# Optimization experiments

Hardware: AMD Instinct MI355X
Metric: run time of the kernel (lower is better)

Reference implementation:

```python
import jax, jax.numpy as jnp
import numpy as np
import math

B, S, H = 8, 2048, 512
DI, DS, DC, DR = 1024, 16, 4, 32   # d_inner, d_state, d_conv, dt_rank
NL, V, NLAB = 8, 32000, 2


def _ln(x, g, b, eps=1e-12):
    mu = jnp.mean(x, -1, keepdims=True)
    var = jnp.mean((x - mu) ** 2, -1, keepdims=True)
    return g * (x - mu) / jnp.sqrt(var + eps) + b


def _gelu_new(x):
    return 0.5 * x * (1.0 + jnp.tanh(np.sqrt(2.0 / np.pi).astype(np.float32) * (x + 0.044715 * x ** 3)))


def _mamba(xin, Wi, cw, cb, Wx, Wdt, bdt, Alog, Dp, Wo):
    # xin: [B,S,H]
    Bb, L, _ = xin.shape
    xz = jnp.einsum('blh,eh->ble', xin, Wi)          # [B,L,2*DI]
    x, z = xz[..., :DI], xz[..., DI:]
    # causal depthwise conv1d, kernel DC, padding DC-1 truncated to L
    xp = jnp.pad(x, ((0, 0), (DC - 1, 0), (0, 0)))
    xc = sum(cw[:, k] * xp[:, k:k + L, :] for k in range(DC)) + cb
    x = jax.nn.silu(xc)
    xdb = jnp.einsum('bld,rd->blr', x, Wx)           # [B,L,DR+2*DS]
    dt = jax.nn.softplus(jnp.einsum('blr,dr->bld', xdb[..., :DR], Wdt) + bdt)
    Bm = xdb[..., DR:DR + DS]
    Cm = xdb[..., DR + DS:]
    A = -jnp.exp(Alog)                               # [DI,DS]

    def step(h, t):
        dt_t, B_t, C_t, x_t = t                      # [B,DI],[B,DS],[B,DS],[B,DI]
        dA = jnp.exp(dt_t[:, :, None] * A)           # [B,DI,DS]
        h = dA * h + (dt_t * x_t)[:, :, None] * B_t[:, None, :]
        return h, jnp.einsum('bdn,bn->bd', h, C_t)

    tm = lambda a: jnp.swapaxes(a, 0, 1)             # time-major
    h0 = jnp.zeros((Bb, DI, DS), x.dtype)
    _, ys = jax.lax.scan(step, h0, (tm(dt), tm(Bm), tm(Cm), tm(x)))
    y = jnp.swapaxes(ys, 0, 1) + Dp * x
    y = y * jax.nn.silu(z)
    return jnp.einsum('bld,hd->blh', y, Wo)


def _forward(input_ids, gate, age_sex, word_emb, pos_emb2, pe, emb_ln_g, emb_ln_b,
             in_proj_w, conv_w, conv_b, x_proj_w, dt_proj_w, dt_proj_b, A_log, D_param,
             out_proj_w, blk_ln_g, blk_ln_b, dense2_w, dense2_b, male_fc_w, male_fc_b,
             gn_g, gn_b, head_w, head_b):
    emb_in = word_emb[input_ids]                                  # [B,S,H]
    emb = pos_emb2[None, :S] * emb_in + pe[None, :S]
    emb = _ln(emb, emb_ln_g, emb_ln_b)
    seq = gate[:, :, None] * emb
    for l in range(NL):
        h = _mamba(seq, in_proj_w[l], conv_w[l], conv_b[l], x_proj_w[l],
                   dt_proj_w[l], dt_proj_b[l], A_log[l], D_param[l], out_proj_w[l])
        seq = gate[:, :, None] * _ln(h + seq, blk_ln_g[l], blk_ln_b[l])
    # ClassificationHead4
    x = seq * gate[:, :, None]
    pooled = jnp.max(x, axis=1)                                   # AdaptiveMaxPool2d((1,H)) == max over seq
    feat = _gelu_new(pooled @ dense2_w.T + dense2_b)              # [B,512]
    style = jax.nn.elu(age_sex @ male_fc_w.T + male_fc_b)         # [B,1024]
    fg = feat.reshape(feat.shape[0], 4, H // 4)                   # GroupNorm(4, 512)
    mu = jnp.mean(fg, -1, keepdims=True)
    var = jnp.mean((fg - mu) ** 2, -1, keepdims=True)
    gn = ((fg - mu) / jnp.sqrt(var + 1e-5)).reshape(feat.shape[0], H) * gn_g + gn_b
    feature = (1.0 + style[:, :H]) * gn + style[:, H:]
    logits = feature @ head_w.T + head_b
    return logits, gate, feature


def setup_inputs() -> dict:
    key = jax.random.key(0)
    ks = jax.random.split(key, 24)
    n = lambda k, sh, s=0.02: jax.random.normal(k, sh, dtype=jnp.float32) * s
    # sinusoidal position buffer
    pos = np.arange(S)[:, None].astype(np.float32)
    div = np.exp(np.arange(0, H, 2).astype(np.float32) * (-math.log(10000.0) / H))
    pe = np.zeros((S, H), np.float32)
    pe[:, 0::2] = np.sin(pos * div)
    pe[:, 1::2] = np.cos(pos * div)
    A_log = jnp.log(jnp.broadcast_to(jnp.arange(1, DS + 1, dtype=jnp.float32), (NL, DI, DS)))
    return {
        'input_ids': jax.random.randint(ks[0], (B, S), 0, V),
        'gate': jax.random.uniform(ks[1], (B, S), dtype=jnp.float32),
        'age_sex': jax.random.normal(ks[2], (B, 2), dtype=jnp.float32),
        'word_emb': n(ks[3], (V, H)),
        'pos_emb2': 1.0 + n(ks[4], (S, H)),
        'pe': jnp.asarray(pe),
        'emb_ln_g': jnp.ones((H,), jnp.float32),
        'emb_ln_b': jnp.zeros((H,), jnp.float32),
        'in_proj_w': n(ks[5], (NL, 2 * DI, H)),
        'conv_w': n(ks[6], (NL, DI, DC), 0.1),
        'conv_b': jnp.zeros((NL, DI), jnp.float32),
        'x_proj_w': n(ks[7], (NL, DR + 2 * DS, DI)),
        'dt_proj_w': n(ks[8], (NL, DI, DR), 0.1),
        'dt_proj_b': n(ks[9], (NL, DI), 0.1),
        'A_log': A_log,
        'D_param': jnp.ones((NL, DI), jnp.float32),
        'out_proj_w': n(ks[10], (NL, H, DI)),
        'blk_ln_g': jnp.ones((NL, H), jnp.float32),
        'blk_ln_b': jnp.zeros((NL, H), jnp.float32),
        'dense2_w': n(ks[11], (512, H)),
        'dense2_b': jnp.zeros((512,), jnp.float32),
        'male_fc_w': n(ks[12], (2 * H, 2)),
        'male_fc_b': jnp.zeros((2 * H,), jnp.float32),
        'gn_g': jnp.ones((512,), jnp.float32),
        'gn_b': jnp.zeros((512,), jnp.float32),
        'head_w': n(ks[13], (NLAB, 512)),
        'head_b': jnp.zeros((NLAB,), jnp.float32),
    }


def reference(input_ids, gate, age_sex, word_emb, pos_emb2, pe, emb_ln_g, emb_ln_b,
              in_proj_w, conv_w, conv_b, x_proj_w, dt_proj_w, dt_proj_b, A_log, D_param,
              out_proj_w, blk_ln_g, blk_ln_b, dense2_w, dense2_b, male_fc_w, male_fc_b,
              gn_g, gn_b, head_w, head_b):
    return _forward(input_ids, gate, age_sex, word_emb, pos_emb2, pe, emb_ln_g, emb_ln_b,
                    in_proj_w, conv_w, conv_b, x_proj_w, dt_proj_w, dt_proj_b, A_log, D_param,
                    out_proj_w, blk_ln_g, blk_ln_b, dense2_w, dense2_b, male_fc_w, male_fc_b,
                    gn_g, gn_b, head_w, head_b)
```

## Files before the change

kernel.cpp:

```cpp
#include <hip/hip_runtime.h>
#include <hip/hip_bf16.h>
#include <hip/hip_fp16.h>
#include <math.h>

#define B_ 8
#define S_ 2048
#define H_ 512
#define DI_ 1024
#define DS_ 16
#define DC_ 4
#define DR_ 32
#define NL_ 8
#define PF_ 4

typedef __hip_bfloat16 bf16;
typedef short bf16x8 __attribute__((ext_vector_type(8)));
typedef float f32x4 __attribute__((ext_vector_type(4)));
typedef float f32x16 __attribute__((ext_vector_type(16)));
typedef unsigned short u16x8 __attribute__((ext_vector_type(8)));

static __device__ __forceinline__ float wred_sum(float v) {
#pragma unroll
  for (int o = 32; o; o >>= 1) v += __shfl_down(v, o, 64);
  return v;
}
static __device__ __forceinline__ float bf2f(unsigned short u) {
  return __uint_as_float(((unsigned)u) << 16);
}
static __device__ __forceinline__ float h2f(unsigned short u) {
  __half_raw r;
  r.x = u;
  return __half2float(r);
}
static __device__ __forceinline__ void st1(float* p, float v) { *p = v; }
static __device__ __forceinline__ void st1(bf16* p, float v) { *p = __float2bfloat16(v); }
static __device__ __forceinline__ void st1(__half* p, float v) { *p = __float2half(v); }
static __device__ __forceinline__ unsigned short f2bfu(float v) {
  bf16 b = __float2bfloat16(v);
  unsigned short u;
  __builtin_memcpy(&u, &b, 2);
  return u;
}

static __device__ __forceinline__ void gl_lds16(const unsigned short* g,
                                                unsigned short* l) {
  __builtin_amdgcn_global_load_lds(
      (const __attribute__((address_space(1))) void*)g,
      (__attribute__((address_space(3))) void*)l, 16, 0, 0);
}

static __device__ __forceinline__ f32x16 ld_c16(const float* p) {
  return *(const __attribute__((address_space(4))) f32x16*)p;
}

template <bool FAST>
static __device__ __forceinline__ void decay16(float dt, const float* A,
                                               float* p) {
  if constexpr (FAST) {
    float q = __expf(-dt);
    float q2 = q * q, q3 = q2 * q, q4 = q2 * q2;
    p[0] = q; p[1] = q2; p[2] = q3; p[3] = q4;
    p[4] = q4 * q; p[5] = q4 * q2; p[6] = q4 * q3;
    float q8 = q4 * q4;
    p[7] = q8;
#pragma unroll
    for (int n = 0; n < 8; n++) p[8 + n] = q8 * p[n];
  } else {
#pragma unroll
    for (int n = 0; n < 16; n++) p[n] = __expf(dt * A[n]);
  }
}

template <int BM, int BN, int ACT, typename TC>
__global__ void __launch_bounds__((BM / 64) * (BN / 64) * 64) k_mfma(
    const unsigned short* __restrict__ X, int lda,
    const unsigned short* __restrict__ W, int ldb,
    const float* __restrict__ bias, TC* __restrict__ C, long ldc, int K,
    unsigned short* __restrict__ dtbf) {
  constexpr int NW = (BM / 64) * (BN / 64);
  constexpr int WN = BN / 64;
  constexpr int SEGS = (BM + BN) / 16;
  __shared__ unsigned short As[BM * 32];
  __shared__ unsigned short Bs[BN * 32];
  int tid = threadIdx.x;
  int wave = tid >> 6, lane = tid & 63;
  int wm = wave / WN, wn = wave % WN;
  long row0 = (long)blockIdx.y * BM;
  long col0 = (long)blockIdx.x * BN;
  int srow = lane >> 2;
  int kchunk = (lane & 3) ^ (srow & 3);
  f32x4 acc[4][4] = {};
  for (int k0 = 0; k0 < K; k0 += 32) {
#pragma unroll
    for (int s = wave; s < SEGS; s += NW) {
      if (s < BM / 16) {
        const unsigned short* g =
            X + (row0 + s * 16 + srow) * (long)lda + k0 + kchunk * 8;
        gl_lds16(g, &As[s * 16 * 32]);
      } else {
        int s2 = s - BM / 16;
        const unsigned short* g =
            W + (col0 + s2 * 16 + srow) * (long)ldb + k0 + kchunk * 8;
        gl_lds16(g, &Bs[s2 * 16 * 32]);
      }
    }
    __syncthreads();
    int fr = lane & 15;
    int slot = (lane >> 4) ^ (lane & 3);
    bf16x8 af[4], bfr[4];
#pragma unroll
    for (int i = 0; i < 4; i++)
      af[i] = *(const bf16x8*)&As[(wm * 64 + i * 16 + fr) * 32 + slot * 8];
#pragma unroll
    for (int j = 0; j < 4; j++)
      bfr[j] = *(const bf16x8*)&Bs[(wn * 64 + j * 16 + fr) * 32 + slot * 8];
#pragma unroll
    for (int i = 0; i < 4; i++)
#pragma unroll
      for (int j = 0; j < 4; j++)
        acc[i][j] = __builtin_amdgcn_mfma_f32_16x16x32_bf16(af[i], bfr[j],
                                                            acc[i][j], 0, 0, 0);
    __syncthreads();
  }
#pragma unroll
  for (int i = 0; i < 4; i++) {
#pragma unroll
    for (int j = 0; j < 4; j++) {
      long rbase = row0 + wm * 64 + i * 16 + ((lane >> 4) << 2);
      long c = col0 + wn * 64 + j * 16 + (lane & 15);
#pragma unroll
      for (int reg = 0; reg < 4; reg++) {
        float v = acc[i][j][reg];
        long r = rbase + reg;
        if constexpr (ACT == 2) {
          if (c < 32) st1((bf16*)&dtbf[r * 32 + c], v);
          else st1((float*)&C[r * ldc + (c - 32)], v);
        } else {
          if constexpr (ACT == 1) {
            v += bias[c];
            v = fmaxf(v, 0.f) + log1pf(__expf(-fabsf(v)));
          }
          st1(&C[r * ldc + c], v);
        }
      }
    }
  }
}

__global__ void k_convert4(const float* __restrict__ s0, int n0,
                           const float* __restrict__ s1, int n1,
                           const float* __restrict__ s2, int n2,
                           const float* __restrict__ s3, int n3,
                           bf16* __restrict__ d0, bf16* __restrict__ d1,
                           bf16* __restrict__ d2, bf16* __restrict__ d3) {
  int i = blockIdx.x * 256 + threadIdx.x;
  int t0 = n0 >> 2, t1 = t0 + (n1 >> 2), t2 = t1 + (n2 >> 2), t3 = t2 + (n3 >> 2);
  const float* s;
  bf16* d;
  int loc;
  if (i < t0) { s = s0; d = d0; loc = i; }
  else if (i < t1) { s = s1; d = d1; loc = i - t0; }
  else if (i < t2) { s = s2; d = d2; loc = i - t1; }
  else if (i < t3) { s = s3; d = d3; loc = i - t2; }
  else return;
  float4 v = ((const float4*)s)[loc];
  bf16* o = d + (long)loc * 4;
  st1(o + 0, v.x); st1(o + 1, v.y); st1(o + 2, v.z); st1(o + 3, v.w);
}

__global__ void k_embed(const int* __restrict__ ids, const float* __restrict__ gate,
                        const float* __restrict__ wemb, const float* __restrict__ pos2,
                        const float* __restrict__ pe, const float* __restrict__ g,
                        const float* __restrict__ bta, bf16* __restrict__ seq) {
  int row = blockIdx.x;
  int s = row % S_;
  int t = threadIdx.x;
  int id = ids[row];
  float v[2];
#pragma unroll
  for (int i = 0; i < 2; i++) {
    int h = t + i * 256;
    v[i] = pos2[s * H_ + h] * wemb[(long)id * H_ + h] + pe[s * H_ + h];
  }
  float lsum = v[0] + v[1];
  float lsq = v[0] * v[0] + v[1] * v[1];
  __shared__ float smA[4], smB[4];
  int lane = t & 63, w = t >> 6;
  lsum = wred_sum(lsum);
  lsq = wred_sum(lsq);
  if (!lane) { smA[w] = lsum; smB[w] = lsq; }
  __syncthreads();
  float tot = smA[0] + smA[1] + smA[2] + smA[3];
  float totq = smB[0] + smB[1] + smB[2] + smB[3];
  float mu = tot * (1.f / H_);
  float var = totq * (1.f / H_) - mu * mu;
  float inv = rsqrtf(fmaxf(var, 0.f) + 1e-12f);
  float gt = gate[row];
#pragma unroll
  for (int i = 0; i < 2; i++) {
    int h = t + i * 256;
    st1(&seq[(long)row * H_ + h], gt * (g[h] * (v[i] - mu) * inv + bta[h]));
  }
}

__global__ void __launch_bounds__(256) k_conv(const bf16* __restrict__ xz,
                                              const float* __restrict__ cw,
                                              const float* __restrict__ cb,
                                              bf16* __restrict__ xc) {
  __shared__ float cwL[8 * 512];
  __shared__ float cbL[8 * 128];
  int tid = threadIdx.x;
#pragma unroll
  for (int m = 0; m < 4; m++) {
    int dd = m * 256 + tid;
    float4 v = ((const float4*)cw)[dd];
    int e = dd & 7, a = dd >> 3;
    *(float4*)&cwL[e * 512 + (((a + e) & 127) << 2)] = v;
  }
  {
    float4 v = ((const float4*)cb)[tid];
#pragma unroll
    for (int m = 0; m < 4; m++) {
      int dd = tid * 4 + m;
      int e = dd & 7, a = dd >> 3;
      cbL[e * 128 + ((a + e) & 127)] = ((const float*)&v)[m];
    }
  }
  __syncthreads();
  long idx = ((long)blockIdx.x * 256 + tid) * 8;
  int d0 = (int)(idx & 1023);
  int A = d0 >> 3;
  long bt = idx >> 10;
  int t = (int)(bt & 2047);
  const unsigned short* xbase = (const unsigned short*)xz + (bt - t) * 2048 + d0;
  f32x4 wk[8];
  float acc[8];
#pragma unroll
  for (int e = 0; e < 8; e++) {
    wk[e] = *(const f32x4*)&cwL[e * 512 + (((A + e) & 127) << 2)];
    acc[e] = cbL[e * 128 + ((A + e) & 127)];
  }
#pragma unroll
  for (int k = 0; k < 4; k++) {
    int ts = t + k - 3;
    if (ts >= 0) {
      u16x8 xv = *(const u16x8*)&xbase[(long)ts * 2048];
#pragma unroll
      for (int e = 0; e < 8; e++) acc[e] += wk[e][k] * bf2f(xv[e]);
    }
  }
  u16x8 ov;
#pragma unroll
  for (int e = 0; e < 8; e++) {
    float s = acc[e] / (1.f + __expf(-acc[e]));
    ov[e] = f2bfu(s);
  }
  *(u16x8*)((unsigned short*)xc + idx) = ov;
}

__global__ void __launch_bounds__(64) k_scan(
    bf16* __restrict__ xzb, const bf16* __restrict__ xc,
    const float* __restrict__ xdb, const float* __restrict__ Alog,
    const float* __restrict__ Dp) {
  int idx = blockIdx.x * 64 + threadIdx.x;
  int half = idx & 1;
  int p = idx >> 1;
  int d = p & 1023;
  int b = p >> 10;
  int n0 = half * 8;
  float A[8];
#pragma unroll
  for (int n = 0; n < 8; n++) A[n] = -__expf(Alog[d * 16 + n0 + n]);
  float Dd = Dp[d];
  float h[8] = {0, 0, 0, 0, 0, 0, 0, 0};
  const __half* dtb = (const __half*)xzb + (long)b * S_ * 2048 + d;
  const unsigned short* xb = (const unsigned short*)xc + (long)b * S_ * DI_ + d;
  const unsigned short* zb = (const unsigned short*)xzb + (long)b * S_ * 2048 + DI_ + d;
  const float* bcb = xdb + (long)b * S_ * 32 + n0;
  bf16* yb = xzb + (long)b * S_ * 2048 + d;
  float dt_c = __half2float(dtb[0]);
  float x_c = bf2f(xb[0]);
  float z_c = bf2f(zb[0]);
  float Bc[8], Cc[8];
#pragma unroll
  for (int n = 0; n < 8; n++) { Bc[n] = bcb[n]; Cc[n] = bcb[16 + n]; }
  for (int t = 0; t < S_; t++) {
    float dt_n = 0.f, x_n = 0.f, z_n = 0.f, Bn[8], Cn[8];
#pragma unroll
    for (int n = 0; n < 8; n++) { Bn[n] = 0.f; Cn[n] = 0.f; }
    if (t + 1 < S_) {
      long o = (long)(t + 1);
      dt_n = __half2float(dtb[o * 2048]);
      x_n = bf2f(xb[o * DI_]);
      z_n = bf2f(zb[o * 2048]);
      const float* bc = bcb + o * 32;
#pragma unroll
      for (int n = 0; n < 8; n++) { Bn[n] = bc[n]; Cn[n] = bc[16 + n]; }
    }
    float dx = dt_c * x_c;
    float yacc = 0.f;
#pragma unroll
    for (int n = 0; n < 8; n++) {
      float hn = __expf(dt_c * A[n]) * h[n] + dx * Bc[n];
      h[n] = hn;
      yacc += hn * Cc[n];
    }
    yacc += __shfl_xor(yacc, 1, 64);
    if (!half) {
      float sz = z_c / (1.f + __expf(-z_c));
      st1(&yb[(long)t * 2048], (yacc + Dd * x_c) * sz);
    }
    dt_c = dt_n; x_c = x_n; z_c = z_n;
#pragma unroll
    for (int n = 0; n < 8; n++) { Bc[n] = Bn[n]; Cc[n] = Cn[n]; }
  }
}

template <int LCv, bool FAST>
static __device__ __forceinline__ void scanA_body16(
    const __half* dtb, const unsigned short* xb, const float* bcb,
    const float* A, int t0, float* h, float& sd) {
  float dtv[PF_], xv[PF_];
  f32x16 bv[2];
#pragma unroll
  for (int i = 0; i < PF_; i++) {
    long o = t0 + i;
    dtv[i] = __half2float(dtb[o * 2048]);
    xv[i] = bf2f(xb[o * DI_]);
  }
#pragma unroll
  for (int i = 0; i < 2; i++) bv[i] = ld_c16(bcb + (long)(t0 + i) * 32);
  for (int t = 0; t < LCv; t += PF_) {
#pragma unroll
    for (int u = 0; u < PF_; u++) {
      float dt_c = dtv[u], x_c = xv[u];
      f32x16 Bv = bv[u & 1];
      long ov = t0 + t + u + PF_;
      dtv[u] = __half2float(dtb[ov * 2048]);
      xv[u] = bf2f(xb[ov * DI_]);
      bv[u & 1] = ld_c16(bcb + (long)(t0 + t + u + 2) * 32);
      sd += dt_c;
      float dx = dt_c * x_c;
      float p[16];
      decay16<FAST>(dt_c, A, p);
#pragma unroll
      for (int n = 0; n < 16; n++) h[n] = p[n] * h[n] + dx * Bv[n];
    }
  }
}

template <int NCv>
__global__ void __launch_bounds__(256) k_scanA(
    const bf16* __restrict__ xzb, const bf16* __restrict__ xc,
    const float* __restrict__ xdb, const float* __restrict__ Alog,
    __half* __restrict__ hf, __half* __restrict__ sdt) {
  constexpr int LCv = S_ / NCv;
  int bx = blockIdx.x;
  int c = bx >> 5;
  int b = (bx >> 2) & 7;
  int d = ((bx & 3) << 8) + threadIdx.x;
  int p = (b << 10) + d;
  float A[16];
  bool fast = true;
#pragma unroll
  for (int n = 0; n < 16; n++) {
    A[n] = -__expf(Alog[d * 16 + n]);
    fast = fast && (fabsf(A[n] + (float)(n + 1)) < 1e-3f);
  }
  const __half* dtb = (const __half*)xzb + (long)b * S_ * 2048 + d;
  const unsigned short* xb = (const unsigned short*)xc + (long)b * S_ * DI_ + d;
  const float* bcb = xdb + (long)b * S_ * 32;
  int t0 = c * LCv;
  float h[16] = {};
  float sd = 0.f;
  if (fast) scanA_body16<LCv, true>(dtb, xb, bcb, A, t0, h, sd);
  else scanA_body16<LCv, false>(dtb, xb, bcb, A, t0, h, sd);
  __half* ho = hf + ((long)c * 8192 + p) * 16;
#pragma unroll
  for (int n = 0; n < 16; n++) st1(&ho[n], h[n]);
  st1(&sdt[c * 8192 + p], sd);
}

template <int NCv>
__global__ void __launch_bounds__(256) k_scanB(
    const float* __restrict__ Alog, __half* __restrict__ hf,
    const __half* __restrict__ sdt) {
  constexpr int M = NCv - 1;
  int i = blockIdx.x * 256 + threadIdx.x;
  int n = i & 15;
  int p = i >> 4;
  int d = p & 1023;
  float An = -__expf(Alog[d * 16 + n]);
  float sdv[8], hjv[8];
#pragma unroll
  for (int k = 0; k < 8; k++) {
    int j = k < M ? k : M - 1;
    sdv[k] = h2f(((const unsigned short*)sdt)[j * 8192 + p]);
    hjv[k] = h2f(((const unsigned short*)hf)[((long)j * 8192 + p) * 16 + n]);
  }
  float H = 0.f;
  for (int j = 0; j < M; j++) {
    float sd = sdv[j & 7], hj = hjv[j & 7];
    int jn = j + 8;
    if (jn > M - 1) jn = M - 1;
    sdv[j & 7] = h2f(((const unsigned short*)sdt)[jn * 8192 + p]);
    hjv[j & 7] = h2f(((const unsigned short*)hf)[((long)jn * 8192 + p) * 16 + n]);
    H = __expf(sd * An) * H + hj;
    st1(&hf[((long)j * 8192 + p) * 16 + n], H);
  }
}

template <bool FAST>
static __device__ __forceinline__ void step16(float dt, float x, float z,
                                              const f32x16& B, const f32x16& C,
                                              const float* A, float Dd,
                                              float* h, bf16* yout) {
  float p[16];
  decay16<FAST>(dt, A, p);
  float dx = dt * x;
  float y0 = 0.f, y1 = 0.f, y2 = 0.f, y3 = 0.f;
#pragma unroll
  for (int n = 0; n < 16; n += 4) {
    float h0 = p[n + 0] * h[n + 0] + dx * B[n + 0];
    float h1 = p[n + 1] * h[n + 1] + dx * B[n + 1];
    float h2 = p[n + 2] * h[n + 2] + dx * B[n + 2];
    float h3 = p[n + 3] * h[n + 3] + dx * B[n + 3];
    h[n + 0] = h0; h[n + 1] = h1; h[n + 2] = h2; h[n + 3] = h3;
    y0 += h0 * C[n + 0];
    y1 += h1 * C[n + 1];
    y2 += h2 * C[n + 2];
    y3 += h3 * C[n + 3];
  }
  float yacc = (y0 + y1) + (y2 + y3);
  float sz = z / (1.f + __expf(-z));
  st1(yout, (yacc + Dd * x) * sz);
}

template <int LCv, bool FAST>
static __device__ __forceinline__ void scanC_body16(
    const __half* dtb, const unsigned short* xb, const unsigned short* zb,
    const float* bcb, bf16* yb, const float* A, int t0, float Dd, float* h) {
  float dtv[PF_], xv[PF_], zv[PF_];
  f32x16 bv[2], cv[2];
#pragma unroll
  for (int i = 0; i < PF_; i++) {
    long o = t0 + i;
    dtv[i] = __half2float(dtb[o * 2048]);
    xv[i] = bf2f(xb[o * DI_]);
    zv[i] = bf2f(zb[o * 2048]);
  }
#pragma unroll
  for (int i = 0; i < 2; i++) {
    bv[i] = ld_c16(bcb + (long)(t0 + i) * 32);
    cv[i] = ld_c16(bcb + (long)(t0 + i) * 32 + 16);
  }
  for (int t = 0; t < LCv - PF_; t += PF_) {
#pragma unroll
    for (int u = 0; u < PF_; u++) {
      float dt_c = dtv[u], x_c = xv[u], z_c = zv[u];
      f32x16 Bv = bv[u & 1], Cv = cv[u & 1];
      long ov = t0 + t + u + PF_;
      dtv[u] = __half2float(dtb[ov * 2048]);
      xv[u] = bf2f(xb[ov * DI_]);
      zv[u] = bf2f(zb[ov * 2048]);
      long os = t0 + t + u + 2;
      bv[u & 1] = ld_c16(bcb + os * 32);
      cv[u & 1] = ld_c16(bcb + os * 32 + 16);
      step16<FAST>(dt_c, x_c, z_c, Bv, Cv, A, Dd, h,
                   yb + (long)(t0 + t + u) * 2048);
    }
  }
#pragma unroll
  for (int u = 0; u < PF_; u++) {
    int tt = LCv - PF_ + u;
    f32x16 Bv, Cv;
    if (u < 2) {
      Bv = bv[u];
      Cv = cv[u];
    } else {
      Bv = ld_c16(bcb + (long)(t0 + tt) * 32);
      Cv = ld_c16(bcb + (long)(t0 + tt) * 32 + 16);
    }
    step16<FAST>(dtv[u], xv[u], zv[u], Bv, Cv, A, Dd, h,
                 yb + (long)(t0 + tt) * 2048);
  }
}

template <int NCv>
__global__ void __launch_bounds__(256) k_scanC(
    bf16* __restrict__ xzb, const bf16* __restrict__ xc,
    const float* __restrict__ xdb, const float* __restrict__ Alog,
    const float* __restrict__ Dp, const __half* __restrict__ hf,
    const __half* __restrict__ sdt) {
  constexpr int LCv = S_ / NCv;
  int bx = blockIdx.x;
  int c = bx >> 5;
  int b = (bx >> 2) & 7;
  int d = ((bx & 3) << 8) + threadIdx.x;
  int p = (b << 10) + d;
  float A[16];
  bool fast = true;
#pragma unroll
  for (int n = 0; n < 16; n++) {
    A[n] = -__expf(Alog[d * 16 + n]);
    fast = fast && (fabsf(A[n] + (float)(n + 1)) < 1e-3f);
  }
  float Dd = Dp[d];
  float h[16] = {};
  if (c > 0) {
    const unsigned short* hs =
        (const unsigned short*)hf + ((long)(c - 1) * 8192 + p) * 16;
    u16x8 a = *(const u16x8*)hs;
    u16x8 b2 = *(const u16x8*)(hs + 8);
#pragma unroll
    for (int n = 0; n < 8; n++) { h[n] = h2f(a[n]); h[8 + n] = h2f(b2[n]); }
  }
  const __half* dtb = (const __half*)xzb + (long)b * S_ * 2048 + d;
  const unsigned short* xb = (const unsigned short*)xc + (long)b * S_ * DI_ + d;
  const unsigned short* zb =
      (const unsigned short*)xzb + (long)b * S_ * 2048 + DI_ + d;
  const float* bcb = xdb + (long)b * S_ * 32;
  bf16* yb = xzb + (long)b * S_ * 2048 + d;
  int t0 = c * LCv;
  if (fast) scanC_body16<LCv, true>(dtb, xb, zb, bcb, yb, A, t0, Dd, h);
  else scanC_body16<LCv, false>(dtb, xb, zb, bcb, yb, A, t0, Dd, h);
}

__global__ void k_resid_ln(const bf16* __restrict__ hb, const float* __restrict__ gate,
                           const float* __restrict__ g, const float* __restrict__ bta,
                           bf16* __restrict__ seq) {
  int row = blockIdx.x;
  int t = threadIdx.x;
  float v[2];
#pragma unroll
  for (int i = 0; i < 2; i++) {
    int h = t + i * 256;
    v[i] = bf2f(((const unsigned short*)hb)[(long)row * H_ + h]) +
           bf2f(((const unsigned short*)seq)[(long)row * H_ + h]);
  }
  float lsum = v[0] + v[1];
  float lsq = v[0] * v[0] + v[1] * v[1];
  __shared__ float smA[4], smB[4];
  int lane = t & 63, w = t >> 6;
  lsum = wred_sum(lsum);
  lsq = wred_sum(lsq);
  if (!lane) { smA[w] = lsum; smB[w] = lsq; }
  __syncthreads();
  float tot = smA[0] + smA[1] + smA[2] + smA[3];
  float totq = smB[0] + smB[1] + smB[2] + smB[3];
  float mu = tot * (1.f / H_);
  float var = totq * (1.f / H_) - mu * mu;
  float inv = rsqrtf(fmaxf(var, 0.f) + 1e-12f);
  float gt = gate[row];
#pragma unroll
  for (int i = 0; i < 2; i++) {
    int h = t + i * 256;
    st1(&seq[(long)row * H_ + h], gt * (g[h] * (v[i] - mu) * inv + bta[h]));
  }
}

__global__ void __launch_bounds__(64) k_pool1(const bf16* __restrict__ seq,
                                              const float* __restrict__ gate,
                                              float* __restrict__ part) {
  int blk = blockIdx.x;
  int b = blk >> 5, c = blk & 31;
  int h0 = threadIdx.x * 8;
  float m[8];
#pragma unroll
  for (int e = 0; e < 8; e++) m[e] = -3.4e38f;
  long r0 = (long)b * S_ + c * 64;
#pragma unroll 4
  for (int i = 0; i < 64; i++) {
    long r = r0 + i;
    u16x8 v = *(const u16x8*)&((const unsigned short*)seq)[r * H_ + h0];
    float g = gate[r];
#pragma unroll
    for (int e = 0; e < 8; e++) m[e] = fmaxf(m[e], bf2f(v[e]) * g);
  }
  float* o = part + ((long)b * 32 + c) * H_ + h0;
#pragma unroll
  for (int e = 0; e < 8; e++) o[e] = m[e];
}
__global__ void k_pool2(const float* __restrict__ part, float* __restrict__ pooled) {
  int idx = blockIdx.x * 256 + threadIdx.x;
  int b = idx >> 9, h = idx & 511;
  float m = -3.4e38f;
#pragma unroll
  for (int c = 0; c < 32; c++) m = fmaxf(m, part[((long)b * 32 + c) * H_ + h]);
  pooled[idx] = m;
}

__global__ void k_feat(const float* __restrict__ pooled, const float* __restrict__ W2,
                       const float* __restrict__ b2, float* __restrict__ feat) {
  int b = blockIdx.x;
  int j = threadIdx.x;
  __shared__ float ps[512];
  ps[j] = pooled[b * 512 + j];
  __syncthreads();
  float acc = b2[j];
  const float4* wr = (const float4*)(W2 + (long)j * 512);
  const float4* p4 = (const float4*)ps;
  for (int k = 0; k < 128; k++) {
    float4 a = p4[k], bb = wr[k];
    acc += a.x * bb.x + a.y * bb.y + a.z * bb.z + a.w * bb.w;
  }
  float x = acc;
  float u = 0.7978845608028654f * (x + 0.044715f * x * x * x);
  feat[b * 512 + j] = 0.5f * x * (1.f + tanhf(u));
}

__global__ void k_head(const float* __restrict__ feat, const float* __restrict__ age_sex,
                       const float* __restrict__ mw, const float* __restrict__ mb,
                       const float* __restrict__ gng, const float* __restrict__ gnb,
                       const float* __restrict__ hw, const float* __restrict__ hb,
                       float* __restrict__ out) {
  int b = blockIdx.x;
  int j = threadIdx.x;
  float f = feat[b * 512 + j];
  __shared__ float sA[8], sB[8];
  int lane = j & 63, w = j >> 6;
  float s1 = wred_sum(f);
  float s2 = wred_sum(f * f);
  if (!lane) { sA[w] = s1; sB[w] = s2; }
  __syncthreads();
  int g = j >> 7;
  float tot = sA[2 * g] + sA[2 * g + 1];
  float totq = sB[2 * g] + sB[2 * g + 1];
  float mu = tot * (1.f / 128.f);
  float var = totq * (1.f / 128.f) - mu * mu;
  float gn = (f - mu) * rsqrtf(fmaxf(var, 0.f) + 1e-5f) * gng[j] + gnb[j];
  float a0 = age_sex[b * 2], a1 = age_sex[b * 2 + 1];
  float sa = a0 * mw[j * 2] + a1 * mw[j * 2 + 1] + mb[j];
  sa = sa > 0.f ? sa : (__expf(sa) - 1.f);
  int j2 = 512 + j;
  float sb = a0 * mw[j2 * 2] + a1 * mw[j2 * 2 + 1] + mb[j2];
  sb = sb > 0.f ? sb : (__expf(sb) - 1.f);
  float feature = (1.f + sa) * gn + sb;
  out[16 + 16384 + b * 512 + j] = feature;
  float l0 = feature * hw[j];
  float l1 = feature * hw[512 + j];
  __syncthreads();
  l0 = wred_sum(l0);
  l1 = wred_sum(l1);
  if (!lane) { sA[w] = l0; sB[w] = l1; }
  __syncthreads();
  if (j == 0) {
    float t0 = 0.f, t1 = 0.f;
#pragma unroll
    for (int i = 0; i < 8; i++) { t0 += sA[i]; t1 += sB[i]; }
    out[b * 2 + 0] = t0 + hb[0];
    out[b * 2 + 1] = t1 + hb[1];
  }
}

__global__ void k_copy(const float* __restrict__ src, float* __restrict__ dst, int n) {
  int i = blockIdx.x * 256 + threadIdx.x;
  if (i < n) dst[i] = src[i];
}

extern "C" void kernel_launch(void* const* d_in, const int* in_sizes, int n_in,
                              void* d_out, int out_size, void* d_ws, size_t ws_size,
                              hipStream_t stream) {
  const int* ids = (const int*)d_in[0];
  const float* gate = (const float*)d_in[1];
  const float* age_sex = (const float*)d_in[2];
  const float* word_emb = (const float*)d_in[3];
  const float* pos_emb2 = (const float*)d_in[4];
  const float* pe = (const float*)d_in[5];
  const float* emb_ln_g = (const float*)d_in[6];
  const float* emb_ln_b = (const float*)d_in[7];
  const float* in_proj_w = (const float*)d_in[8];
  const float* conv_w = (const float*)d_in[9];
  const float* conv_b = (const float*)d_in[10];
  const float* x_proj_w = (const float*)d_in[11];
  const float* dt_proj_w = (const float*)d_in[12];
  const float* dt_proj_b = (const float*)d_in[13];
  const float* A_log = (const float*)d_in[14];
  const float* D_param = (const float*)d_in[15];
  const float* out_proj_w = (const float*)d_in[16];
  const float* blk_ln_g = (const float*)d_in[17];
  const float* blk_ln_b = (const float*)d_in[18];
  const float* dense2_w = (const float*)d_in[19];
  const float* dense2_b = (const float*)d_in[20];
  const float* male_fc_w = (const float*)d_in[21];
  const float* male_fc_b = (const float*)d_in[22];
  const float* gn_g = (const float*)d_in[23];
  const float* gn_b = (const float*)d_in[24];
  const float* head_w = (const float*)d_in[25];
  const float* head_b = (const float*)d_in[26];
  float* out = (float*)d_out;

  char* w = (char*)d_ws;
  bf16* seq = (bf16*)(w);
  bf16* xz = (bf16*)(w + 16777216);
  bf16* xc = (bf16*)(w + 83886080);
  float* xdb = (float*)(w + 117440512);
  bf16* wo_b = (bf16*)(w + 119537664);
  bf16* wi_b = (bf16*)(w + 120586240);
  bf16* wx_b = (bf16*)(w + 122683392);
  bf16* wdt_b = (bf16*)(w + 122814464);
  bf16* xdt = (bf16*)(w + 122880000);
  __half* hf = (__half*)(w + 120586240);
  float* part = (float*)(w + 120586240);
  float* pooled = (float*)(w + 121110528);
  float* featp = (float*)(w + 121126912);

  const size_t base = 120586240;
  int NC = 0;
  if (ws_size >= base + (size_t)63 * 8192 * 34) NC = 64;
  else if (ws_size >= base + (size_t)31 * 8192 * 34) NC = 32;
  else if (ws_size >= base + (size_t)15 * 8192 * 34) NC = 16;
  __half* sdt = (__half*)(w + base + (size_t)(NC > 0 ? NC - 1 : 0) * 8192 * 32);

  k_embed<<<B_ * S_, 256, 0, stream>>>(ids, gate, word_emb, pos_emb2, pe, emb_ln_g,
                                       emb_ln_b, seq);

  const int nWi = 2 * DI_ * H_;
  const int nWx = 64 * DI_;
  const int nWdt = DI_ * DR_;
  const int nWo = H_ * DI_;
  const int cvt_blocks = (nWi + nWx + nWdt + nWo) / 4 / 256;

  for (int l = 0; l < NL_; l++) {
    const float* Wi = in_proj_w + (long)l * nWi;
    const float* cw = conv_w + (long)l * DI_ * DC_;
    const float* cb = conv_b + (long)l * DI_;
    const float* Wx = x_proj_w + (long)l * nWx;
    const float* Wdt = dt_proj_w + (long)l * nWdt;
    const float* bdt = dt_proj_b + (long)l * DI_;
    const float* Al = A_log + (long)l * DI_ * DS_;
    const float* Dl = D_param + (long)l * DI_;
    const float* Wo = out_proj_w + (long)l * nWo;
    const float* bg = blk_ln_g + (long)l * H_;
    const float* bb = blk_ln_b + (long)l * H_;

    k_convert4<<<cvt_blocks, 256, 0, stream>>>(Wi, nWi, Wx, nWx, Wdt, nWdt, Wo, nWo,
                                               wi_b, wx_b, wdt_b, wo_b);

    k_mfma<128, 128, 0, bf16><<<dim3(16, 128), 256, 0, stream>>>(
        (const unsigned short*)seq, H_, (const unsigned short*)wi_b, H_, nullptr,
        xz, 2048, H_, nullptr);
    k_conv<<<(B_ * S_ * DI_) / 8 / 256, 256, 0, stream>>>(xz, cw, cb, xc);
    k_mfma<64, 64, 2, float><<<dim3(1, 256), 64, 0, stream>>>(
        (const unsigned short*)xc, DI_, (const unsigned short*)wx_b, DI_, nullptr,
        xdb, 32, DI_, (unsigned short*)xdt);
    k_mfma<128, 128, 1, __half><<<dim3(8, 128), 256, 0, stream>>>(
        (const unsigned short*)xdt, 32, (const unsigned short*)wdt_b, DR_, bdt,
        (__half*)xz, 2048, DR_, nullptr);
    if (NC == 64) {
      k_scanA<64><<<63 * 32, 256, 0, stream>>>(xz, xc, xdb, Al, hf, sdt);
      k_scanB<64><<<512, 256, 0, stream>>>(Al, hf, sdt);
      k_scanC<64><<<64 * 32, 256, 0, stream>>>(xz, xc, xdb, Al, Dl, hf, sdt);
    } else if (NC == 32) {
      k_scanA<32><<<31 * 32, 256, 0, stream>>>(xz, xc, xdb, Al, hf, sdt);
      k_scanB<32><<<512, 256, 0, stream>>>(Al, hf, sdt);
      k_scanC<32><<<32 * 32, 256, 0, stream>>>(xz, xc, xdb, Al, Dl, hf, sdt);
    } else if (NC == 16) {
      k_scanA<16><<<15 * 32, 256, 0, stream>>>(xz, xc, xdb, Al, hf, sdt);
      k_scanB<16><<<512, 256, 0, stream>>>(Al, hf, sdt);
      k_scanC<16><<<16 * 32, 256, 0, stream>>>(xz, xc, xdb, Al, Dl, hf, sdt);
    } else {
      k_scan<<<256, 64, 0, stream>>>(xz, xc, xdb, Al, Dl);
    }
    k_mfma<128, 128, 0, bf16><<<dim3(4, 128), 256, 0, stream>>>(
        (const unsigned short*)xz, 2048, (const unsigned short*)wo_b, DI_, nullptr,
        xc, H_, DI_, nullptr);
    k_resid_ln<<<B_ * S_, 256, 0, stream>>>(xc, gate, bg, bb, seq);
  }

  k_pool1<<<B_ * 32, 64, 0, stream>>>(seq, gate, part);
  k_pool2<<<16, 256, 0, stream>>>(part, pooled);
  k_feat<<<B_, 512, 0, stream>>>(pooled, dense2_w, dense2_b, featp);
  k_head<<<B_, 512, 0, stream>>>(featp, age_sex, male_fc_w, male_fc_b, gn_g, gn_b,
                                 head_w, head_b, out);
  k_copy<<<(B_ * S_ + 255) / 256, 256, 0, stream>>>(gate, out + 16, B_ * S_);
}
```

Measured before the change: 2.711 ms.

## Fuse SiLU(z) into in_proj GEMM epilogue and pack scan state as float2

The SiLU gate on z is moved into the in_proj GEMM epilogue (ACT==3, columns >= 1024), so the scan kernels read pre-activated z and skip the per-step exp and division. The scan state and decay factors are held as float2 vectors so the compiler can emit packed FP32 multiply/FMA instructions on the CDNA hardware. The trade-off is that z is rounded to bf16 after SiLU rather than before, which changes rounding slightly. The epilogue also pays a small extra cost for the activation on half of the columns.

Measured after the change: 2.518 ms. -7.1%, faster.

```diff
diff --git a/kernel.cpp b/kernel.cpp
--- a/kernel.cpp
+++ b/kernel.cpp
@@ -15,6 +15,7 @@
 
 typedef __hip_bfloat16 bf16;
 typedef short bf16x8 __attribute__((ext_vector_type(8)));
+typedef float f32x2 __attribute__((ext_vector_type(2)));
 typedef float f32x4 __attribute__((ext_vector_type(4)));
 typedef float f32x16 __attribute__((ext_vector_type(16)));
 typedef unsigned short u16x8 __attribute__((ext_vector_type(8)));
@@ -68,6 +69,32 @@
   } else {
 #pragma unroll
     for (int n = 0; n < 16; n++) p[n] = __expf(dt * A[n]);
+  }
+}
+
+template <bool FAST>
+static __device__ __forceinline__ void decay16p(float dt, const float* A,
+                                                f32x2* P) {
+  if constexpr (FAST) {
+    float q = __expf(-dt);
+    float q2 = q * q;
+    f32x2 Q2 = {q2, q2};
+    f32x2 Q4 = Q2 * Q2;
+    f32x2 Q8 = Q4 * Q4;
+    P[0][0] = q; P[0][1] = q2;
+    P[1] = P[0] * Q2;
+    P[2] = P[0] * Q4;
+    P[3] = P[1] * Q4;
+    P[4] = P[0] * Q8;
+    P[5] = P[1] * Q8;
+    P[6] = P[2] * Q8;
+    P[7] = P[3] * Q8;
+  } else {
+#pragma unroll
+    for (int k = 0; k < 8; k++) {
+      P[k][0] = __expf(dt * A[2 * k]);
+      P[k][1] = __expf(dt * A[2 * k + 1]);
+    }
   }
 }
 
@@ -140,6 +167,9 @@
             v += bias[c];
             v = fmaxf(v, 0.f) + log1pf(__expf(-fabsf(v)));
           }
+          if constexpr (ACT == 3) {
+            if (c >= 1024) v = v / (1.f + __expf(-v));
+          }
           st1(&C[r * ldc + c], v);
         }
       }
@@ -307,8 +337,7 @@
     }
     yacc += __shfl_xor(yacc, 1, 64);
     if (!half) {
-      float sz = z_c / (1.f + __expf(-z_c));
-      st1(&yb[(long)t * 2048], (yacc + Dd * x_c) * sz);
+      st1(&yb[(long)t * 2048], (yacc + Dd * x_c) * z_c);
     }
     dt_c = dt_n; x_c = x_n; z_c = z_n;
 #pragma unroll
@@ -319,7 +348,7 @@
 template <int LCv, bool FAST>
 static __device__ __forceinline__ void scanA_body16(
     const __half* dtb, const unsigned short* xb, const float* bcb,
-    const float* A, int t0, float* h, float& sd) {
+    const float* A, int t0, f32x2* h, float& sd) {
   float dtv[PF_], xv[PF_];
   f32x16 bv[2];
 #pragma unroll
@@ -341,10 +370,12 @@
       bv[u & 1] = ld_c16(bcb + (long)(t0 + t + u + 2) * 32);
       sd += dt_c;
       float dx = dt_c * x_c;
-      float p[16];
-      decay16<FAST>(dt_c, A, p);
-#pragma unroll
-      for (int n = 0; n < 16; n++) h[n] = p[n] * h[n] + dx * Bv[n];
+      f32x2 dx2 = {dx, dx};
+      f32x2 P[8];
+      decay16p<FAST>(dt_c, A, P);
+      const f32x2* Bp = (const f32x2*)&Bv;
+#pragma unroll
+      for (int k = 0; k < 8; k++) h[k] = P[k] * h[k] + dx2 * Bp[k];
     }
   }
 }
@@ -371,13 +402,16 @@
   const unsigned short* xb = (const unsigned short*)xc + (long)b * S_ * DI_ + d;
   const float* bcb = xdb + (long)b * S_ * 32;
   int t0 = c * LCv;
-  float h[16] = {};
+  f32x2 h[8] = {};
   float sd = 0.f;
   if (fast) scanA_body16<LCv, true>(dtb, xb, bcb, A, t0, h, sd);
   else scanA_body16<LCv, false>(dtb, xb, bcb, A, t0, h, sd);
   __half* ho = hf + ((long)c * 8192 + p) * 16;
 #pragma unroll
-  for (int n = 0; n < 16; n++) st1(&ho[n], h[n]);
+  for (int k = 0; k < 8; k++) {
+    st1(&ho[2 * k], h[k][0]);
+    st1(&ho[2 * k + 1], h[k][1]);
+  }
   st1(&sdt[c * 8192 + p], sd);
 }
 
@@ -411,35 +445,38 @@
 }
 
 template <bool FAST>
-static __device__ __forceinline__ void step16(float dt, float x, float z,
-                                              const f32x16& B, const f32x16& C,
+static __device__ __forceinline__ void step16(float dt, float x, float zs,
+                                              const f32x16& Bv, const f32x16& Cv,
                                               const float* A, float Dd,
-                                              float* h, bf16* yout) {
-  float p[16];
-  decay16<FAST>(dt, A, p);
+                                              f32x2* h, bf16* yout) {
+  f32x2 P[8];
+  decay16p<FAST>(dt, A, P);
   float dx = dt * x;
-  float y0 = 0.f, y1 = 0.f, y2 = 0.f, y3 = 0.f;
-#pragma unroll
-  for (int n = 0; n < 16; n += 4) {
-    float h0 = p[n + 0] * h[n + 0] + dx * B[n + 0];
-    float h1 = p[n + 1] * h[n + 1] + dx * B[n + 1];
-    float h2 = p[n + 2] * h[n + 2] + dx * B[n + 2];
-    float h3 = p[n + 3] * h[n + 3] + dx * B[n + 3];
-    h[n + 0] = h0; h[n + 1] = h1; h[n + 2] = h2; h[n + 3] = h3;
-    y0 += h0 * C[n + 0];
-    y1 += h1 * C[n + 1];
-    y2 += h2 * C[n + 2];
-    y3 += h3 * C[n + 3];
-  }
-  float yacc = (y0 + y1) + (y2 + y3);
-  float sz = z / (1.f + __expf(-z));
-  st1(yout, (yacc + Dd * x) * sz);
+  f32x2 dx2 = {dx, dx};
+  const f32x2* Bp = (const f32x2*)&Bv;
+  const f32x2* Cp = (const f32x2*)&Cv;
+  f32x2 Y0 = {0.f, 0.f}, Y1 = {0.f, 0.f}, Y2 = {0.f, 0.f}, Y3 = {0.f, 0.f};
+#pragma unroll
+  for (int k = 0; k < 8; k += 4) {
+    f32x2 h0 = P[k + 0] * h[k + 0] + dx2 * Bp[k + 0];
+    f32x2 h1 = P[k + 1] * h[k + 1] + dx2 * Bp[k + 1];
+    f32x2 h2 = P[k + 2] * h[k + 2] + dx2 * Bp[k + 2];
+    f32x2 h3 = P[k + 3] * h[k + 3] + dx2 * Bp[k + 3];
+    h[k + 0] = h0; h[k + 1] = h1; h[k + 2] = h2; h[k + 3] = h3;
+    Y0 += h0 * Cp[k + 0];
+    Y1 += h1 * Cp[k + 1];
+    Y2 += h2 * Cp[k + 2];
+    Y3 += h3 * Cp[k + 3];
+  }
+  f32x2 Yv = (Y0 + Y1) + (Y2 + Y3);
+  float yacc = Yv[0] + Yv[1];
+  st1(yout, (yacc + Dd * x) * zs);
 }
 
 template <int LCv, bool FAST>
 static __device__ __forceinline__ void scanC_body16(
     const __half* dtb, const unsigned short* xb, const unsigned short* zb,
-    const float* bcb, bf16* yb, const float* A, int t0, float Dd, float* h) {
+    const float* bcb, bf16* yb, const float* A, int t0, float Dd, f32x2* h) {
   float dtv[PF_], xv[PF_], zv[PF_];
   f32x16 bv[2], cv[2];
 #pragma unroll
@@ -506,14 +543,19 @@
     fast = fast && (fabsf(A[n] + (float)(n + 1)) < 1e-3f);
   }
   float Dd = Dp[d];
-  float h[16] = {};
+  f32x2 h[8] = {};
   if (c > 0) {
     const unsigned short* hs =
         (const unsigned short*)hf + ((long)(c - 1) * 8192 + p) * 16;
     u16x8 a = *(const u16x8*)hs;
     u16x8 b2 = *(const u16x8*)(hs + 8);
 #pragma unroll
-    for (int n = 0; n < 8; n++) { h[n] = h2f(a[n]); h[8 + n] = h2f(b2[n]); }
+    for (int k = 0; k < 4; k++) {
+      h[k][0] = h2f(a[2 * k]);
+      h[k][1] = h2f(a[2 * k + 1]);
+      h[4 + k][0] = h2f(b2[2 * k]);
+      h[4 + k][1] = h2f(b2[2 * k + 1]);
+    }
   }
   const __half* dtb = (const __half*)xzb + (long)b * S_ * 2048 + d;
   const unsigned short* xb = (const unsigned short*)xc + (long)b * S_ * DI_ + d;
@@ -737,7 +779,7 @@
     k_convert4<<<cvt_blocks, 256, 0, stream>>>(Wi, nWi, Wx, nWx, Wdt, nWdt, Wo, nWo,
                                                wi_b, wx_b, wdt_b, wo_b);
 
-    k_mfma<128, 128, 0, bf16><<<dim3(16, 128), 256, 0, stream>>>(
+    k_mfma<128, 128, 3, bf16><<<dim3(16, 128), 256, 0, stream>>>(
         (const unsigned short*)seq, H_, (const unsigned short*)wi_b, H_, nullptr,
         xz, 2048, H_, nullptr);
     k_conv<<<(B_ * S_ * DI_) / 8 / 256, 256, 0, stream>>>(xz, cw, cb, xc);
```
